# Kernel optimization log

Hardware: AMD Instinct MI355X
Metric: run time of the kernel (lower is better)

Reference implementation:

```python
import jax, jax.numpy as jnp
import numpy as np

B, L, D, N, F, V, NL, NS = 2, 1024, 768, 16, 3072, 32000, 4, 3
EPS = 1e-5


def _layernorm(x, g, b):
    m = x.mean(-1, keepdims=True)
    v = ((x - m) ** 2).mean(-1, keepdims=True)
    return (x - m) / jnp.sqrt(v + EPS) * g + b


def _ssm_sublayer(x, cw, A_log, WB, WC, Wdt, dtb, Dsk):
    # x: [B,L,D]; causal depthwise conv, kernel_size=3
    xp = jnp.pad(x, ((0, 0), (2, 0), (0, 0)))
    u = xp[:, :-2] * cw[:, 0] + xp[:, 1:-1] * cw[:, 1] + xp[:, 2:] * cw[:, 2]
    u = jax.nn.silu(u)
    dt = jax.nn.softplus(jnp.einsum('bld,de->ble', u, Wdt) + dtb)   # [B,L,D]
    Bm = jnp.einsum('bld,dn->bln', u, WB)                           # [B,L,N]
    Cm = jnp.einsum('bld,dn->bln', u, WC)                           # [B,L,N]
    A = -jnp.exp(A_log)                                             # [D,N]

    def step(h, t):
        dt_t, u_t, b_t, c_t = t                                     # [B,D],[B,D],[B,N],[B,N]
        h = jnp.exp(dt_t[..., None] * A) * h + (dt_t * u_t)[..., None] * b_t[:, None, :]
        y = jnp.einsum('bdn,bn->bd', h, c_t)
        return h, y

    h0 = jnp.zeros((x.shape[0], x.shape[2], A.shape[1]), x.dtype)
    _, ys = jax.lax.scan(step, h0, (dt.transpose(1, 0, 2), u.transpose(1, 0, 2),
                                    Bm.transpose(1, 0, 2), Cm.transpose(1, 0, 2)))
    return ys.transpose(1, 0, 2) + Dsk * u


def setup_inputs() -> dict:
    key = jax.random.key(0)
    ks = jax.random.split(key, 16)
    g = lambda k, shape, s=0.02: jax.random.normal(k, shape, jnp.float32) * s
    inp = {
        'x': jax.random.randint(ks[0], (B, L), 0, V),
        'emb': g(ks[1], (V, D)),
        'conv_w': g(ks[2], (NL, NS, D, 3), 0.2),
        'A_log': jnp.log(jnp.tile(jnp.arange(1, N + 1, dtype=jnp.float32), (NL, NS, D, 1))),
        'W_B': g(ks[3], (NL, NS, D, N)),
        'W_C': g(ks[4], (NL, NS, D, N)),
        'W_dt': g(ks[5], (NL, NS, D, D)),
        'dt_bias': jnp.full((NL, NS, D), -4.0, jnp.float32),
        'D_skip': jnp.ones((NL, NS, D), jnp.float32),
        'ffn_W1': g(ks[6], (NL, D, F)),
        'ffn_b1': jnp.zeros((NL, F), jnp.float32),
        'ffn_W2': g(ks[7], (NL, F, D)),
        'ffn_b2': jnp.zeros((NL, D), jnp.float32),
        'norm_g': jnp.ones((D,), jnp.float32),
        'norm_b': jnp.zeros((D,), jnp.float32),
        'out_W': g(ks[8], (D, V)),
        'out_b': jnp.zeros((V,), jnp.float32),
    }
    return inp


def reference(x, emb, conv_w, A_log, W_B, W_C, W_dt, dt_bias, D_skip,
              ffn_W1, ffn_b1, ffn_W2, ffn_b2, norm_g, norm_b, out_W, out_b):
    h = emb[x]                                                      # [B,L,D]
    for l in range(NL):
        for s in range(NS):
            h = h + _ssm_sublayer(h, conv_w[l, s], A_log[l, s], W_B[l, s],
                                  W_C[l, s], W_dt[l, s], dt_bias[l, s], D_skip[l, s])
        f = jax.nn.gelu(jnp.einsum('bld,df->blf', h, ffn_W1[l]) + ffn_b1[l], approximate=False)
        h = h + jnp.einsum('blf,fd->bld', f, ffn_W2[l]) + ffn_b2[l]
    h = _layernorm(h, norm_g, norm_b)
    logits = jnp.einsum('bld,dv->blv', h, out_W) + out_b            # [B,L,V]
    return logits
```

## Files before the change

### kernel.cpp

```cpp
#include <hip/hip_runtime.h>
#include <hip/hip_bf16.h>
#include <math.h>

#define BB 2
#define LL 1024
#define DD 768
#define NN 16
#define FF 3072
#define VV 32000
#define NLL 4
#define NSS 3
#define BL (BB*LL)
#define CHK 64
#define CLEN (LL/CHK)

typedef __bf16 bf16x8 __attribute__((ext_vector_type(8)));
typedef float f32x4 __attribute__((ext_vector_type(4)));
typedef short short8 __attribute__((ext_vector_type(8)));
typedef short short4v __attribute__((ext_vector_type(4)));

typedef __attribute__((address_space(1))) const void gconst_t;
typedef __attribute__((address_space(3))) void lds_t;

__device__ __forceinline__ void g2l16(const void* g, void* l) {
  __builtin_amdgcn_global_load_lds((gconst_t*)g, (lds_t*)l, 16, 0, 0);
}



__global__ __launch_bounds__(256) void k_embed(
    const int* __restrict__ x, const float* __restrict__ emb,
    float* __restrict__ h) {
  int gid = blockIdx.x * 256 + threadIdx.x;
  int row = gid / 192;
  int g = (gid - row * 192) * 4;
  int idx = x[row];
  *(float4*)&h[(size_t)row * DD + g] =
      *(const float4*)&emb[(size_t)idx * DD + g];
}

__global__ __launch_bounds__(256) void k_conv(
    const float* __restrict__ h, const float* __restrict__ cw,
    __hip_bfloat16* __restrict__ ub) {
  int gid = blockIdx.x * 256 + threadIdx.x;
  int row = gid / 192;
  int g = gid - row * 192;
  int d0 = g * 4;
  int l = row & (LL - 1);
  float4 h0 = *(const float4*)&h[(size_t)row * DD + d0];
  float4 h1, h2;
  if (l >= 1) h1 = *(const float4*)&h[(size_t)(row - 1) * DD + d0];
  else { h1.x = h1.y = h1.z = h1.w = 0.f; }
  if (l >= 2) h2 = *(const float4*)&h[(size_t)(row - 2) * DD + d0];
  else { h2.x = h2.y = h2.z = h2.w = 0.f; }
  const float* hp0 = (const float*)&h0;
  const float* hp1 = (const float*)&h1;
  const float* hp2 = (const float*)&h2;
  alignas(8) __hip_bfloat16 o[4];
  #pragma unroll
  for (int i = 0; i < 4; ++i) {
    int d = d0 + i;
    float v = hp2[i] * cw[d * 3 + 0] + hp1[i] * cw[d * 3 + 1] + hp0[i] * cw[d * 3 + 2];
    float sv = v / (1.f + __expf(-v));
    o[i] = __float2bfloat16(sv);
  }
  *(short4v*)&ub[(size_t)row * DD + d0] = *(short4v*)o;
}

__global__ __launch_bounds__(256) void k_layernorm(
    const float* __restrict__ x, const float* __restrict__ g,
    const float* __restrict__ bta, __hip_bfloat16* __restrict__ o) {
  int row = blockIdx.x;
  const float* xr = x + (size_t)row * DD;
  int tid = threadIdx.x;
  float v1 = xr[tid], v2 = xr[tid + 256], v3 = xr[tid + 512];
  float s = v1 + v2 + v3;
  float sq = v1 * v1 + v2 * v2 + v3 * v3;
  #pragma unroll
  for (int m = 1; m < 64; m <<= 1) {
    s  += __shfl_xor(s, m);
    sq += __shfl_xor(sq, m);
  }
  __shared__ float ss[4], sqs[4];
  if ((tid & 63) == 0) { ss[tid >> 6] = s; sqs[tid >> 6] = sq; }
  __syncthreads();
  s  = ss[0] + ss[1] + ss[2] + ss[3];
  sq = sqs[0] + sqs[1] + sqs[2] + sqs[3];
  float mean = s * (1.f / DD);
  float var  = sq * (1.f / DD) - mean * mean;
  float rstd = rsqrtf(var + 1e-5f);
  o[(size_t)row * DD + tid]       = __float2bfloat16((v1 - mean) * rstd * g[tid]       + bta[tid]);
  o[(size_t)row * DD + tid + 256] = __float2bfloat16((v2 - mean) * rstd * g[tid + 256] + bta[tid + 256]);
  o[(size_t)row * DD + tid + 512] = __float2bfloat16((v3 - mean) * rstd * g[tid + 512] + bta[tid + 512]);
}

#define S1 1728
#define S2 1740
#define S3 4044
#define S4 6348
#define SEND 12348

__global__ __launch_bounds__(256) void k_wconv_all(
    const float* __restrict__ Wdt, const float* __restrict__ WB,
    const float* __restrict__ WC, const float* __restrict__ W1,
    const float* __restrict__ W2, const float* __restrict__ Wout,
    __hip_bfloat16* __restrict__ WTdt, __hip_bfloat16* __restrict__ WT1,
    __hip_bfloat16* __restrict__ WT2, __hip_bfloat16* __restrict__ WTlog) {
  __shared__ float T[64][65];
  int bid = blockIdx.x;
  int tid = threadIdx.x;

  if (bid >= S1 && bid < S2) {
    int sub = bid - S1;
    const float* WBp = WB + (size_t)sub * DD * NN;
    const float* WCp = WC + (size_t)sub * DD * NN;
    __hip_bfloat16* dst = WTdt + (size_t)sub * 832 * DD;
    for (int e = tid; e < 64 * DD; e += 256) {
      int r = e / DD, k = e - (e / DD) * DD;
      float v = 0.f;
      if (r < 16)      v = WBp[(size_t)k * NN + r];
      else if (r < 32) v = WCp[(size_t)k * NN + (r - 16)];
      dst[(size_t)(768 + r) * DD + k] = __float2bfloat16(v);
    }
    return;
  }

  const float* W; __hip_bfloat16* WT;
  int K, N, n0, k0;
  if (bid < S1) {
    int sub = bid / 144, t = bid % 144;
    W = Wdt + (size_t)sub * DD * DD; WT = WTdt + (size_t)sub * 832 * DD;
    K = DD; N = DD; n0 = (t % 12) * 64; k0 = (t / 12) * 64;
  } else if (bid < S3) {
    int idx = bid - S2, l = idx / 576, t = idx % 576;
    W = W1 + (size_t)l * DD * FF; WT = WT1 + (size_t)l * FF * DD;
    K = DD; N = FF; n0 = (t % 48) * 64; k0 = (t / 48) * 64;
  } else if (bid < S4) {
    int idx = bid - S3, l = idx / 576, t = idx % 576;
    W = W2 + (size_t)l * FF * DD; WT = WT2 + (size_t)l * DD * FF;
    K = FF; N = DD; n0 = (t % 12) * 64; k0 = (t / 12) * 64;
  } else {
    int t = bid - S4;
    W = Wout; WT = WTlog;
    K = DD; N = VV; n0 = (t % 500) * 64; k0 = (t / 500) * 64;
  }

  {
    int r0 = tid >> 4, c4 = (tid & 15) * 4;
    #pragma unroll
    for (int i = 0; i < 4; ++i) {
      int r = r0 + 16 * i;
      float4 v = *(const float4*)&W[(size_t)(k0 + r) * N + n0 + c4];
      T[r][c4 + 0] = v.x;
      T[r][c4 + 1] = v.y;
      T[r][c4 + 2] = v.z;
      T[r][c4 + 3] = v.w;
    }
  }
  __syncthreads();
  {
    int c8 = tid & 7;
    #pragma unroll
    for (int j = 0; j < 2; ++j) {
      int n_l = (tid >> 3) + 32 * j;
      alignas(16) __hip_bfloat16 ox[8];
      #pragma unroll
      for (int i = 0; i < 8; ++i)
        ox[i] = __float2bfloat16(T[c8 * 8 + i][n_l]);
      *(short8*)&WT[(size_t)(n0 + n_l) * K + k0 + c8 * 8] = *(short8*)ox;
    }
  }
}

__device__ __forceinline__ float softplus_f(float x) {
  return (x > 20.f) ? x : log1pf(__expf(x));
}
__device__ __forceinline__ float gelu_f(float x) {
  return 0.5f * x * (1.f + erff(x * 0.70710678118654752f));
}

__global__ __launch_bounds__(256) void k_gemm_ffn1(
    const __hip_bfloat16* __restrict__ A, const __hip_bfloat16* __restrict__ BT,
    const float* __restrict__ bias, __hip_bfloat16* __restrict__ Cb) {
  __shared__ __align__(16) __hip_bfloat16 As[128 * 64];
  __shared__ __align__(16) __hip_bfloat16 Bs[128 * 64];
  const int tid = threadIdx.x;
  const int lane = tid & 63, wid = tid >> 6;
  int wg = (blockIdx.x & 7) * 48 + (blockIdx.x >> 3);
  int tn = wg % 24, tm = wg / 24;
  const int bm = tm * 128, bn = tn * 128;
  const int wm = wid >> 1, wn = wid & 1;
  const int sr = lane >> 3;
  const int sks = (((lane & 7) ^ (lane >> 3)) & 7) * 8;
  const int N = FF, K = DD;

  f32x4 acc[4][4] = {};

  for (int k0 = 0; k0 < K; k0 += 64) {
    __syncthreads();
    #pragma unroll
    for (int cc = 0; cc < 4; ++cc) {
      int ch = wid * 4 + cc;
      int row = ch * 8 + sr;
      g2l16(A  + (size_t)(bm + row) * K + k0 + sks, &As[ch * 512]);
      g2l16(BT + (size_t)(bn + row) * K + k0 + sks, &Bs[ch * 512]);
    }
    __syncthreads();
    #pragma unroll
    for (int kk = 0; kk < 2; ++kk) {
      int koff = (((kk * 4 + (lane >> 4)) ^ (lane & 7)) & 7) * 8;
      bf16x8 af[4], bfr[4];
      #pragma unroll
      for (int m = 0; m < 4; ++m)
        af[m] = *(const bf16x8*)&As[(wm * 64 + m * 16 + (lane & 15)) * 64 + koff];
      #pragma unroll
      for (int n = 0; n < 4; ++n)
        bfr[n] = *(const bf16x8*)&Bs[(wn * 64 + n * 16 + (lane & 15)) * 64 + koff];
      #pragma unroll
      for (int m = 0; m < 4; ++m)
        #pragma unroll
        for (int n = 0; n < 4; ++n)
          acc[m][n] = __builtin_amdgcn_mfma_f32_16x16x32_bf16(af[m], bfr[n], acc[m][n], 0, 0, 0);
    }
  }

  const int crow0 = (lane >> 4) * 4;
  const int ccol = lane & 15;
  #pragma unroll
  for (int m = 0; m < 4; ++m) {
    #pragma unroll
    for (int n = 0; n < 4; ++n) {
      int col = bn + wn * 64 + n * 16 + ccol;
      float bv = bias[col];
      #pragma unroll
      for (int j = 0; j < 4; ++j) {
        int row = bm + wm * 64 + m * 16 + crow0 + j;
        Cb[(size_t)row * N + col] = __float2bfloat16(gelu_f(acc[m][n][j] + bv));
      }
    }
  }
}

__global__ __launch_bounds__(256) void k_gemm_dtbc64(
    const __hip_bfloat16* __restrict__ A, const __hip_bfloat16* __restrict__ BT,
    const float* __restrict__ dtbias, __hip_bfloat16* __restrict__ dtbb,
    float* __restrict__ Bm, float* __restrict__ Cm) {
  __shared__ __align__(16) __hip_bfloat16 As[64 * 64];
  __shared__ __align__(16) __hip_bfloat16 Bs[64 * 64];
  const int tid = threadIdx.x;
  const int lane = tid & 63, wid = tid >> 6;
  int wg = (blockIdx.x & 7) * 52 + (blockIdx.x >> 3);
  int tn = wg % 13, tm = wg / 13;
  const int bm = tm * 64, bn = tn * 64;
  const int wm = wid >> 1, wn = wid & 1;
  const int sr = lane >> 3;
  const int sks = (((lane & 7) ^ (lane >> 3)) & 7) * 8;

  f32x4 acc[2][2] = {};

  for (int k0 = 0; k0 < DD; k0 += 64) {
    __syncthreads();
    #pragma unroll
    for (int cc = 0; cc < 2; ++cc) {
      int ch = wid * 2 + cc;
      int row = ch * 8 + sr;
      g2l16(A  + (size_t)(bm + row) * DD + k0 + sks, &As[ch * 512]);
      g2l16(BT + (size_t)(bn + row) * DD + k0 + sks, &Bs[ch * 512]);
    }
    __syncthreads();
    #pragma unroll
    for (int kk = 0; kk < 2; ++kk) {
      int koff = (((kk * 4 + (lane >> 4)) ^ (lane & 7)) & 7) * 8;
      bf16x8 af[2], bfr[2];
      #pragma unroll
      for (int m = 0; m < 2; ++m)
        af[m] = *(const bf16x8*)&As[(wm * 32 + m * 16 + (lane & 15)) * 64 + koff];
      #pragma unroll
      for (int n = 0; n < 2; ++n)
        bfr[n] = *(const bf16x8*)&Bs[(wn * 32 + n * 16 + (lane & 15)) * 64 + koff];
      #pragma unroll
      for (int m = 0; m < 2; ++m)
        #pragma unroll
        for (int n = 0; n < 2; ++n)
          acc[m][n] = __builtin_amdgcn_mfma_f32_16x16x32_bf16(af[m], bfr[n], acc[m][n], 0, 0, 0);
    }
  }

  const int crow0 = (lane >> 4) * 4;
  const int ccol = lane & 15;
  #pragma unroll
  for (int m = 0; m < 2; ++m) {
    #pragma unroll
    for (int n = 0; n < 2; ++n) {
      int col = bn + wn * 32 + n * 16 + ccol;
      if (col >= 800) continue;
      float bv = (col < DD) ? dtbias[col] : 0.f;
      #pragma unroll
      for (int j = 0; j < 4; ++j) {
        int row = bm + wm * 32 + m * 16 + crow0 + j;
        float v = acc[m][n][j] + bv;
        if (col < DD)       dtbb[(size_t)row * DD + col] = __float2bfloat16(softplus_f(v));
        else if (col < 784) Bm[(size_t)row * NN + (col - DD)] = v;
        else                Cm[(size_t)row * NN + (col - 784)] = v;
      }
    }
  }
}

__global__ __launch_bounds__(256) void k_gemm_ffn2s(
    const __hip_bfloat16* __restrict__ A, const __hip_bfloat16* __restrict__ BT,
    const float* __restrict__ bias, float* __restrict__ h) {
  __shared__ __align__(16) __hip_bfloat16 As[64 * 64];
  __shared__ __align__(16) __hip_bfloat16 Bs[64 * 64];
  const int tid = threadIdx.x;
  const int lane = tid & 63, wid = tid >> 6;
  int wg = (blockIdx.x & 7) * 96 + (blockIdx.x >> 3);
  int tile = wg % 384, split = wg / 384;
  int tm = tile % 32, tn = tile / 32;
  const int bm = tm * 64, bn = tn * 64;
  const int wm = wid >> 1, wn = wid & 1;
  const int sr = lane >> 3;
  const int sks = (((lane & 7) ^ (lane >> 3)) & 7) * 8;
  const int kbeg = split * (FF / 2), kend = kbeg + FF / 2;

  f32x4 acc[2][2] = {};

  for (int k0 = kbeg; k0 < kend; k0 += 64) {
    __syncthreads();
    #pragma unroll
    for (int cc = 0; cc < 2; ++cc) {
      int ch = wid * 2 + cc;
      int row = ch * 8 + sr;
      g2l16(A  + (size_t)(bm + row) * FF + k0 + sks, &As[ch * 512]);
      g2l16(BT + (size_t)(bn + row) * FF + k0 + sks, &Bs[ch * 512]);
    }
    __syncthreads();
    #pragma unroll
    for (int kk = 0; kk < 2; ++kk) {
      int koff = (((kk * 4 + (lane >> 4)) ^ (lane & 7)) & 7) * 8;
      bf16x8 af[2], bfr[2];
      #pragma unroll
      for (int m = 0; m < 2; ++m)
        af[m] = *(const bf16x8*)&As[(wm * 32 + m * 16 + (lane & 15)) * 64 + koff];
      #pragma unroll
      for (int n = 0; n < 2; ++n)
        bfr[n] = *(const bf16x8*)&Bs[(wn * 32 + n * 16 + (lane & 15)) * 64 + koff];
      #pragma unroll
      for (int m = 0; m < 2; ++m)
        #pragma unroll
        for (int n = 0; n < 2; ++n)
          acc[m][n] = __builtin_amdgcn_mfma_f32_16x16x32_bf16(af[m], bfr[n], acc[m][n], 0, 0, 0);
    }
  }

  const int crow0 = (lane >> 4) * 4;
  const int ccol = lane & 15;
  #pragma unroll
  for (int m = 0; m < 2; ++m) {
    #pragma unroll
    for (int n = 0; n < 2; ++n) {
      int col = bn + wn * 32 + n * 16 + ccol;
      float bv = (split == 0) ? bias[col] : 0.f;
      #pragma unroll
      for (int j = 0; j < 4; ++j) {
        int row = bm + wm * 32 + m * 16 + crow0 + j;
        unsafeAtomicAdd(&h[(size_t)row * DD + col], acc[m][n][j] + bv);
      }
    }
  }
}

__global__ __launch_bounds__(512) void k_gemm_logits2(
    const __hip_bfloat16* __restrict__ A, const __hip_bfloat16* __restrict__ BT,
    const float* __restrict__ bias, float* __restrict__ C, int M, int N, int K) {
  __shared__ __align__(16) char smem[(256 * 64 + 128 * 64) * 2];
  __hip_bfloat16* As = (__hip_bfloat16*)smem;
  __hip_bfloat16* Bs = (__hip_bfloat16*)(smem + 256 * 64 * 2);
  const int tid = threadIdx.x;
  const int lane = tid & 63, wid = tid >> 6;
  int bid = blockIdx.y * gridDim.x + blockIdx.x;
  int mt = bid & 7, nt = bid >> 3;
  const int bm = mt * 256, bn = nt * 128;
  const int wm = wid >> 1, wn = wid & 1;
  const int sr = lane >> 3;
  const int sks = (((lane & 7) ^ (lane >> 3)) & 7) * 8;

  f32x4 acc[4][4] = {};

  for (int k0 = 0; k0 < K; k0 += 64) {
    __syncthreads();
    #pragma unroll
    for (int r = 0; r < 4; ++r) {
      int ch = r * 8 + wid;
      int row = ch * 8 + sr;
      g2l16(A + (size_t)(bm + row) * K + k0 + sks, &As[ch * 512]);
    }
    #pragma unroll
    for (int r = 0; r < 2; ++r) {
      int ch = r * 8 + wid;
      int row = ch * 8 + sr;
      g2l16(BT + (size_t)(bn + row) * K + k0 + sks, &Bs[ch * 512]);
    }
    __syncthreads();
    #pragma unroll
    for (int kk = 0; kk < 2; ++kk) {
      int koff = (((kk * 4 + (lane >> 4)) ^ (lane & 7)) & 7) * 8;
      bf16x8 af[4], bfr[4];
      #pragma unroll
      for (int m = 0; m < 4; ++m)
        af[m] = *(const bf16x8*)&As[(wm * 64 + m * 16 + (lane & 15)) * 64 + koff];
      #pragma unroll
      for (int n = 0; n < 4; ++n)
        bfr[n] = *(const bf16x8*)&Bs[(wn * 64 + n * 16 + (lane & 15)) * 64 + koff];
      #pragma unroll
      for (int m = 0; m < 4; ++m)
        #pragma unroll
        for (int n = 0; n < 4; ++n)
          acc[m][n] = __builtin_amdgcn_mfma_f32_16x16x32_bf16(af[m], bfr[n], acc[m][n], 0, 0, 0);
    }
  }

  __syncthreads();
  float* eps = (float*)smem + (size_t)wid * 1088;
  const int crow0 = (lane >> 4) * 4;
  const int ccol = lane & 15;
  const int gcolbase = bn + wn * 64;
  #pragma unroll
  for (int m = 0; m < 4; ++m) {
    #pragma unroll
    for (int n = 0; n < 4; ++n) {
      float bv = bias[gcolbase + n * 16 + ccol];
      #pragma unroll
      for (int j = 0; j < 4; ++j)
        eps[(crow0 + j) * 68 + n * 16 + ccol] = acc[m][n][j] + bv;
    }
    int growbase = bm + wm * 64 + m * 16;
    #pragma unroll
    for (int p = 0; p < 2; ++p) {
      int r = (lane >> 3) + 8 * p;
      #pragma unroll
      for (int i = 0; i < 2; ++i) {
        int s4 = (lane & 7) + 8 * i;
        float4 v = *(float4*)&eps[r * 68 + s4 * 4];
        *(float4*)&C[(size_t)(growbase + r) * N + gcolbase + s4 * 4] = v;
      }
    }
  }
}

__global__ __launch_bounds__(256) void k_scan_a(
    const __hip_bfloat16* __restrict__ dt, const __hip_bfloat16* __restrict__ ub,
    const float* __restrict__ Bm, const float* __restrict__ A_log,
    __hip_bfloat16* __restrict__ F, float* __restrict__ SD) {
  int c = blockIdx.x;
  int bd = blockIdx.y;
  int b = bd / 3;
  int d = (bd % 3) * 256 + threadIdx.x;
  float Av[16];
  {
    const float4* al = (const float4*)(A_log + (size_t)d * NN);
    #pragma unroll
    for (int q = 0; q < 4; ++q) {
      float4 v = al[q];
      Av[q * 4 + 0] = -__expf(v.x);
      Av[q * 4 + 1] = -__expf(v.y);
      Av[q * 4 + 2] = -__expf(v.z);
      Av[q * 4 + 3] = -__expf(v.w);
    }
  }
  float h[16];
  #pragma unroll
  for (int n = 0; n < 16; ++n) h[n] = 0.f;
  float sdt = 0.f;
  size_t base = ((size_t)b * LL + (size_t)c * CLEN) * DD + d;
  int row0 = c * CLEN + b * LL;
  #pragma unroll 4
  for (int t = 0; t < CLEN; ++t) {
    float dtv = __bfloat162float(dt[base + (size_t)t * DD]);
    float uv  = __bfloat162float(ub[base + (size_t)t * DD]);
    float Bv[16];
    const float4* bp = (const float4*)(Bm + (size_t)(row0 + t) * NN);
    *(float4*)&Bv[0]  = bp[0];
    *(float4*)&Bv[4]  = bp[1];
    *(float4*)&Bv[8]  = bp[2];
    *(float4*)&Bv[12] = bp[3];
    float du = dtv * uv;
    sdt += dtv;
    #pragma unroll
    for (int n = 0; n < 16; ++n)
      h[n] = __expf(dtv * Av[n]) * h[n] + du * Bv[n];
  }
  alignas(16) __hip_bfloat16 fx[16];
  #pragma unroll
  for (int n = 0; n < 16; ++n) fx[n] = __float2bfloat16(h[n]);
  __hip_bfloat16* fo = F + (((size_t)c * BB + b) * DD + d) * NN;
  *(short8*)&fo[0] = *(short8*)&fx[0];
  *(short8*)&fo[8] = *(short8*)&fx[8];
  SD[((size_t)c * BB + b) * DD + d] = sdt;
}

__global__ __launch_bounds__(256) void k_scan_b(
    const __hip_bfloat16* __restrict__ F, const float* __restrict__ SD,
    const float* __restrict__ A_log, __hip_bfloat16* __restrict__ Hinit) {
  __shared__ float Ls[64 * 17];
  __shared__ float Ho[64 * 17];
  __shared__ float Ss[64];
  int bd = blockIdx.x;
  int b = bd / DD, d = bd % DD;
  int tid = threadIdx.x;
  if (tid < 128) {
    int c = tid >> 1, q = tid & 1;
    alignas(16) __hip_bfloat16 fx[8];
    *(short8*)fx = *(const short8*)(F + (((size_t)c * BB + b) * DD + d) * NN + q * 8);
    #pragma unroll
    for (int i = 0; i < 8; ++i)
      Ls[c * 17 + q * 8 + i] = __bfloat162float(fx[i]);
  }
  if (tid < 64) Ss[tid] = SD[((size_t)tid * BB + b) * DD + d];
  __syncthreads();
  int lane = tid & 63, w = tid >> 6;
  #pragma unroll
  for (int r = 0; r < 4; ++r) {
    int n = w * 4 + r;
    float Av = -__expf(A_log[(size_t)d * NN + n]);
    float Fv = Ls[lane * 17 + n];
    float Dv = __expf(Ss[lane] * Av);
    #pragma unroll
    for (int s = 1; s < 64; s <<= 1) {
      float Fp = __shfl_up(Fv, s);
      float Dp = __shfl_up(Dv, s);
      float nF = Fv + Dv * Fp;
      float nD = Dv * Dp;
      Fv = (lane >= s) ? nF : Fv;
      Dv = (lane >= s) ? nD : Dv;
    }
    float Hi = __shfl_up(Fv, 1);
    if (lane == 0) Hi = 0.f;
    Ho[lane * 17 + n] = Hi;
  }
  __syncthreads();
  if (tid < 128) {
    int c = tid >> 1, q = tid & 1;
    alignas(16) __hip_bfloat16 hx[8];
    #pragma unroll
    for (int i = 0; i < 8; ++i)
      hx[i] = __float2bfloat16(Ho[c * 17 + q * 8 + i]);
    *(short8*)(Hinit + (((size_t)c * BB + b) * DD + d) * NN + q * 8) = *(short8*)hx;
  }
}

__global__ __launch_bounds__(256) void k_scan_c(
    const __hip_bfloat16* __restrict__ dt, const __hip_bfloat16* __restrict__ ub,
    const float* __restrict__ Bm, const float* __restrict__ Cm,
    const float* __restrict__ A_log, const float* __restrict__ Dsk,
    const __hip_bfloat16* __restrict__ Hinit, float* __restrict__ hres,
    __hip_bfloat16* __restrict__ hb, int writeHb) {
  int c = blockIdx.x;
  int bd = blockIdx.y;
  int b = bd / 3;
  int d = (bd % 3) * 256 + threadIdx.x;
  float Av[16];
  {
    const float4* al = (const float4*)(A_log + (size_t)d * NN);
    #pragma unroll
    for (int q = 0; q < 4; ++q) {
      float4 v = al[q];
      Av[q * 4 + 0] = -__expf(v.x);
      Av[q * 4 + 1] = -__expf(v.y);
      Av[q * 4 + 2] = -__expf(v.z);
      Av[q * 4 + 3] = -__expf(v.w);
    }
  }
  float h[16];
  {
    alignas(16) __hip_bfloat16 hx[16];
    const __hip_bfloat16* hi = Hinit + (((size_t)c * BB + b) * DD + d) * NN;
    *(short8*)&hx[0] = *(const short8*)&hi[0];
    *(short8*)&hx[8] = *(const short8*)&hi[8];
    #pragma unroll
    for (int n = 0; n < 16; ++n) h[n] = __bfloat162float(hx[n]);
  }
  float dskip = Dsk[d];
  size_t base = ((size_t)b * LL + (size_t)c * CLEN) * DD + d;
  int row0 = c * CLEN + b * LL;
  #pragma unroll 4
  for (int t = 0; t < CLEN; ++t) {
    float dtv = __bfloat162float(dt[base + (size_t)t * DD]);
    float uv  = __bfloat162float(ub[base + (size_t)t * DD]);
    float Bv[16], Cv[16];
    const float4* bp = (const float4*)(Bm + (size_t)(row0 + t) * NN);
    const float4* cp = (const float4*)(Cm + (size_t)(row0 + t) * NN);
    *(float4*)&Bv[0]  = bp[0];
    *(float4*)&Bv[4]  = bp[1];
    *(float4*)&Bv[8]  = bp[2];
    *(float4*)&Bv[12] = bp[3];
    *(float4*)&Cv[0]  = cp[0];
    *(float4*)&Cv[4]  = cp[1];
    *(float4*)&Cv[8]  = cp[2];
    *(float4*)&Cv[12] = cp[3];
    float du = dtv * uv;
    float y = 0.f;
    #pragma unroll
    for (int n = 0; n < 16; ++n) {
      h[n] = __expf(dtv * Av[n]) * h[n] + du * Bv[n];
      y += h[n] * Cv[n];
    }
    float nh = hres[base + (size_t)t * DD] + y + dskip * uv;
    hres[base + (size_t)t * DD] = nh;
    if (writeHb) hb[base + (size_t)t * DD] = __float2bfloat16(nh);
  }
}

extern "C" void kernel_launch(void* const* d_in, const int* in_sizes, int n_in,
                              void* d_out, int out_size, void* d_ws, size_t ws_size,
                              hipStream_t stream) {
  const int*   x     = (const int*)d_in[0];
  const float* emb   = (const float*)d_in[1];
  const float* convw = (const float*)d_in[2];
  const float* A_log = (const float*)d_in[3];
  const float* W_B   = (const float*)d_in[4];
  const float* W_C   = (const float*)d_in[5];
  const float* W_dt  = (const float*)d_in[6];
  const float* dt_b  = (const float*)d_in[7];
  const float* D_sk  = (const float*)d_in[8];
  const float* W1    = (const float*)d_in[9];
  const float* b1    = (const float*)d_in[10];
  const float* W2    = (const float*)d_in[11];
  const float* b2    = (const float*)d_in[12];
  const float* ng    = (const float*)d_in[13];
  const float* nb    = (const float*)d_in[14];
  const float* Wout  = (const float*)d_in[15];
  const float* bout  = (const float*)d_in[16];
  float* out = (float*)d_out;

  __hip_bfloat16* WTdt = (__hip_bfloat16*)d_out;
  __hip_bfloat16* WT1  = WTdt + (size_t)12 * 832 * DD;
  __hip_bfloat16* WT2  = WT1  + (size_t)NLL * FF * DD;

  char* p = (char*)d_ws;
  auto alloc = [&](size_t bytes) { char* r = p; p += (bytes + 255) & ~(size_t)255; return r; };
  float* h    = (float*)alloc((size_t)BL * DD * 4);
  float* Bm   = (float*)alloc((size_t)BL * NN * 4);
  float* Cm   = (float*)alloc((size_t)BL * NN * 4);
  float* SD   = (float*)alloc((size_t)CHK * BB * DD * 4);
  __hip_bfloat16* dtbb  = (__hip_bfloat16*)alloc((size_t)BL * DD * 2);
  __hip_bfloat16* F     = (__hip_bfloat16*)alloc((size_t)CHK * BB * DD * NN * 2);
  __hip_bfloat16* Hini  = (__hip_bfloat16*)alloc((size_t)CHK * BB * DD * NN * 2);
  __hip_bfloat16* ub    = (__hip_bfloat16*)alloc((size_t)BL * DD * 2);
  __hip_bfloat16* hb    = (__hip_bfloat16*)alloc((size_t)BL * DD * 2);
  __hip_bfloat16* fb    = (__hip_bfloat16*)alloc((size_t)BL * FF * 2);
  __hip_bfloat16* lnb   = (__hip_bfloat16*)alloc((size_t)BL * DD * 2);
  __hip_bfloat16* WTlog = (__hip_bfloat16*)alloc((size_t)VV * DD * 2);

  k_wconv_all<<<SEND, 256, 0, stream>>>(
      W_dt, W_B, W_C, W1, W2, Wout, WTdt, WT1, WT2, WTlog);
  k_embed<<<1536, 256, 0, stream>>>(x, emb, h);

  for (int l = 0; l < NLL; ++l) {
    for (int s = 0; s < NSS; ++s) {
      int ls = l * NSS + s;
      k_conv<<<1536, 256, 0, stream>>>(h, convw + (size_t)ls * DD * 3, ub);
      k_gemm_dtbc64<<<416, 256, 0, stream>>>(
          ub, WTdt + (size_t)ls * 832 * DD, dt_b + (size_t)ls * DD, dtbb, Bm, Cm);
      k_scan_a<<<dim3(CHK, 6), 256, 0, stream>>>(
          dtbb, ub, Bm, A_log + (size_t)ls * DD * NN, F, SD);
      k_scan_b<<<BB * DD, 256, 0, stream>>>(
          F, SD, A_log + (size_t)ls * DD * NN, Hini);
      k_scan_c<<<dim3(CHK, 6), 256, 0, stream>>>(
          dtbb, ub, Bm, Cm, A_log + (size_t)ls * DD * NN, D_sk + (size_t)ls * DD,
          Hini, h, hb, (s == NSS - 1) ? 1 : 0);
    }
    k_gemm_ffn1<<<384, 256, 0, stream>>>(
        hb, WT1 + (size_t)l * FF * DD, b1 + (size_t)l * FF, fb);
    k_gemm_ffn2s<<<768, 256, 0, stream>>>(
        fb, WT2 + (size_t)l * DD * FF, b2 + (size_t)l * DD, h);
  }

  k_layernorm<<<BL, 256, 0, stream>>>(h, ng, nb, lnb);
  k_gemm_logits2<<<dim3(VV / 128, BL / 256), 512, 0, stream>>>(
      lnb, WTlog, bout, out, BL, VV, DD);
}
```

Baseline: 1.119 ms.

## Fuse three chunked-scan kernels into one cooperative kernel with grid syncs

Merges the chunk-local scan, cross-chunk prefix scan, and final scan passes into a single cooperative kernel of 384 blocks separated by grid-wide barriers, replacing two kernel launch boundaries per sublayer. The middle phase is re-mapped so each wavefront handles one (batch, channel) pair with 16 state elements per lane instead of one block per pair. This removes launch overhead and lets A values stay in registers across phases, at the cost of grid.sync overhead and reliance on all blocks being co-resident.

Measured after the change: 3.369 ms. 201% more time.

```diff
diff --git a/kernel.cpp b/kernel.cpp
--- a/kernel.cpp
+++ b/kernel.cpp
@@ -1,6 +1,9 @@
 #include <hip/hip_runtime.h>
 #include <hip/hip_bf16.h>
+#include <hip/hip_cooperative_groups.h>
 #include <math.h>
+
+namespace cg = cooperative_groups;
 
 #define BB 2
 #define LL 1024
@@ -448,14 +451,21 @@
   }
 }
 
-__global__ __launch_bounds__(256) void k_scan_a(
+__global__ __launch_bounds__(256) void k_scan_fused(
     const __hip_bfloat16* __restrict__ dt, const __hip_bfloat16* __restrict__ ub,
-    const float* __restrict__ Bm, const float* __restrict__ A_log,
-    __hip_bfloat16* __restrict__ F, float* __restrict__ SD) {
-  int c = blockIdx.x;
-  int bd = blockIdx.y;
-  int b = bd / 3;
-  int d = (bd % 3) * 256 + threadIdx.x;
+    const float* __restrict__ Bm, const float* __restrict__ Cm,
+    const float* __restrict__ A_log, const float* __restrict__ Dsk,
+    __hip_bfloat16* __restrict__ F, float* __restrict__ SD,
+    __hip_bfloat16* __restrict__ Hinit, float* __restrict__ hres,
+    __hip_bfloat16* __restrict__ hb, int writeHb) {
+  cg::grid_group grid = cg::this_grid();
+  int blk = blockIdx.x;
+  int tid = threadIdx.x;
+  int c = blk & 63;
+  int seg = blk >> 6;
+  int b = seg / 3;
+  int d = (seg % 3) * 256 + tid;
+
   float Av[16];
   {
     const float4* al = (const float4*)(A_log + (size_t)d * NN);
@@ -468,146 +478,136 @@
       Av[q * 4 + 3] = -__expf(v.w);
     }
   }
-  float h[16];
-  #pragma unroll
-  for (int n = 0; n < 16; ++n) h[n] = 0.f;
-  float sdt = 0.f;
-  size_t base = ((size_t)b * LL + (size_t)c * CLEN) * DD + d;
-  int row0 = c * CLEN + b * LL;
-  #pragma unroll 4
-  for (int t = 0; t < CLEN; ++t) {
-    float dtv = __bfloat162float(dt[base + (size_t)t * DD]);
-    float uv  = __bfloat162float(ub[base + (size_t)t * DD]);
-    float Bv[16];
-    const float4* bp = (const float4*)(Bm + (size_t)(row0 + t) * NN);
-    *(float4*)&Bv[0]  = bp[0];
-    *(float4*)&Bv[4]  = bp[1];
-    *(float4*)&Bv[8]  = bp[2];
-    *(float4*)&Bv[12] = bp[3];
-    float du = dtv * uv;
-    sdt += dtv;
-    #pragma unroll
-    for (int n = 0; n < 16; ++n)
-      h[n] = __expf(dtv * Av[n]) * h[n] + du * Bv[n];
-  }
-  alignas(16) __hip_bfloat16 fx[16];
-  #pragma unroll
-  for (int n = 0; n < 16; ++n) fx[n] = __float2bfloat16(h[n]);
-  __hip_bfloat16* fo = F + (((size_t)c * BB + b) * DD + d) * NN;
-  *(short8*)&fo[0] = *(short8*)&fx[0];
-  *(short8*)&fo[8] = *(short8*)&fx[8];
-  SD[((size_t)c * BB + b) * DD + d] = sdt;
-}
-
-__global__ __launch_bounds__(256) void k_scan_b(
-    const __hip_bfloat16* __restrict__ F, const float* __restrict__ SD,
-    const float* __restrict__ A_log, __hip_bfloat16* __restrict__ Hinit) {
-  __shared__ float Ls[64 * 17];
-  __shared__ float Ho[64 * 17];
-  __shared__ float Ss[64];
-  int bd = blockIdx.x;
-  int b = bd / DD, d = bd % DD;
-  int tid = threadIdx.x;
-  if (tid < 128) {
-    int c = tid >> 1, q = tid & 1;
-    alignas(16) __hip_bfloat16 fx[8];
-    *(short8*)fx = *(const short8*)(F + (((size_t)c * BB + b) * DD + d) * NN + q * 8);
-    #pragma unroll
-    for (int i = 0; i < 8; ++i)
-      Ls[c * 17 + q * 8 + i] = __bfloat162float(fx[i]);
-  }
-  if (tid < 64) Ss[tid] = SD[((size_t)tid * BB + b) * DD + d];
-  __syncthreads();
-  int lane = tid & 63, w = tid >> 6;
-  #pragma unroll
-  for (int r = 0; r < 4; ++r) {
-    int n = w * 4 + r;
-    float Av = -__expf(A_log[(size_t)d * NN + n]);
-    float Fv = Ls[lane * 17 + n];
-    float Dv = __expf(Ss[lane] * Av);
-    #pragma unroll
-    for (int s = 1; s < 64; s <<= 1) {
-      float Fp = __shfl_up(Fv, s);
-      float Dp = __shfl_up(Dv, s);
-      float nF = Fv + Dv * Fp;
-      float nD = Dv * Dp;
-      Fv = (lane >= s) ? nF : Fv;
-      Dv = (lane >= s) ? nD : Dv;
-    }
-    float Hi = __shfl_up(Fv, 1);
-    if (lane == 0) Hi = 0.f;
-    Ho[lane * 17 + n] = Hi;
-  }
-  __syncthreads();
-  if (tid < 128) {
-    int c = tid >> 1, q = tid & 1;
-    alignas(16) __hip_bfloat16 hx[8];
-    #pragma unroll
-    for (int i = 0; i < 8; ++i)
-      hx[i] = __float2bfloat16(Ho[c * 17 + q * 8 + i]);
-    *(short8*)(Hinit + (((size_t)c * BB + b) * DD + d) * NN + q * 8) = *(short8*)hx;
-  }
-}
-
-__global__ __launch_bounds__(256) void k_scan_c(
-    const __hip_bfloat16* __restrict__ dt, const __hip_bfloat16* __restrict__ ub,
-    const float* __restrict__ Bm, const float* __restrict__ Cm,
-    const float* __restrict__ A_log, const float* __restrict__ Dsk,
-    const __hip_bfloat16* __restrict__ Hinit, float* __restrict__ hres,
-    __hip_bfloat16* __restrict__ hb, int writeHb) {
-  int c = blockIdx.x;
-  int bd = blockIdx.y;
-  int b = bd / 3;
-  int d = (bd % 3) * 256 + threadIdx.x;
-  float Av[16];
+
   {
-    const float4* al = (const float4*)(A_log + (size_t)d * NN);
-    #pragma unroll
-    for (int q = 0; q < 4; ++q) {
-      float4 v = al[q];
-      Av[q * 4 + 0] = -__expf(v.x);
-      Av[q * 4 + 1] = -__expf(v.y);
-      Av[q * 4 + 2] = -__expf(v.z);
-      Av[q * 4 + 3] = -__expf(v.w);
-    }
-  }
-  float h[16];
+    float hA[16];
+    #pragma unroll
+    for (int n = 0; n < 16; ++n) hA[n] = 0.f;
+    float sdt = 0.f;
+    size_t base = ((size_t)b * LL + (size_t)c * CLEN) * DD + d;
+    int row0 = c * CLEN + b * LL;
+    #pragma unroll 4
+    for (int t = 0; t < CLEN; ++t) {
+      float dtv = __bfloat162float(dt[base + (size_t)t * DD]);
+      float uv  = __bfloat162float(ub[base + (size_t)t * DD]);
+      float Bv[16];
+      const float4* bp = (const float4*)(Bm + (size_t)(row0 + t) * NN);
+      *(float4*)&Bv[0]  = bp[0];
+      *(float4*)&Bv[4]  = bp[1];
+      *(float4*)&Bv[8]  = bp[2];
+      *(float4*)&Bv[12] = bp[3];
+      float du = dtv * uv;
+      sdt += dtv;
+      #pragma unroll
+      for (int n = 0; n < 16; ++n)
+        hA[n] = __expf(dtv * Av[n]) * hA[n] + du * Bv[n];
+    }
+    alignas(16) __hip_bfloat16 fx[16];
+    #pragma unroll
+    for (int n = 0; n < 16; ++n) fx[n] = __float2bfloat16(hA[n]);
+    __hip_bfloat16* fo = F + (((size_t)c * BB + b) * DD + d) * NN;
+    *(short8*)&fo[0] = *(short8*)&fx[0];
+    *(short8*)&fo[8] = *(short8*)&fx[8];
+    SD[((size_t)c * BB + b) * DD + d] = sdt;
+  }
+
+  __threadfence();
+  grid.sync();
+
   {
-    alignas(16) __hip_bfloat16 hx[16];
-    const __hip_bfloat16* hi = Hinit + (((size_t)c * BB + b) * DD + d) * NN;
-    *(short8*)&hx[0] = *(const short8*)&hi[0];
-    *(short8*)&hx[8] = *(const short8*)&hi[8];
-    #pragma unroll
-    for (int n = 0; n < 16; ++n) h[n] = __bfloat162float(hx[n]);
-  }
-  float dskip = Dsk[d];
-  size_t base = ((size_t)b * LL + (size_t)c * CLEN) * DD + d;
-  int row0 = c * CLEN + b * LL;
-  #pragma unroll 4
-  for (int t = 0; t < CLEN; ++t) {
-    float dtv = __bfloat162float(dt[base + (size_t)t * DD]);
-    float uv  = __bfloat162float(ub[base + (size_t)t * DD]);
-    float Bv[16], Cv[16];
-    const float4* bp = (const float4*)(Bm + (size_t)(row0 + t) * NN);
-    const float4* cp = (const float4*)(Cm + (size_t)(row0 + t) * NN);
-    *(float4*)&Bv[0]  = bp[0];
-    *(float4*)&Bv[4]  = bp[1];
-    *(float4*)&Bv[8]  = bp[2];
-    *(float4*)&Bv[12] = bp[3];
-    *(float4*)&Cv[0]  = cp[0];
-    *(float4*)&Cv[4]  = cp[1];
-    *(float4*)&Cv[8]  = cp[2];
-    *(float4*)&Cv[12] = cp[3];
-    float du = dtv * uv;
-    float y = 0.f;
+    int w = tid >> 6, lane = tid & 63;
+    int task = blk * 4 + w;
+    int b2 = task / DD, d2 = task - b2 * DD;
+    float Av2[16];
+    {
+      const float4* al = (const float4*)(A_log + (size_t)d2 * NN);
+      #pragma unroll
+      for (int q = 0; q < 4; ++q) {
+        float4 v = al[q];
+        Av2[q * 4 + 0] = -__expf(v.x);
+        Av2[q * 4 + 1] = -__expf(v.y);
+        Av2[q * 4 + 2] = -__expf(v.z);
+        Av2[q * 4 + 3] = -__expf(v.w);
+      }
+    }
+    float sd = SD[((size_t)lane * BB + b2) * DD + d2];
+    float Fr[16], Hr[16];
+    {
+      alignas(16) __hip_bfloat16 fx[16];
+      const __hip_bfloat16* fp = F + (((size_t)lane * BB + b2) * DD + d2) * NN;
+      *(short8*)&fx[0] = *(const short8*)&fp[0];
+      *(short8*)&fx[8] = *(const short8*)&fp[8];
+      #pragma unroll
+      for (int n = 0; n < 16; ++n) Fr[n] = __bfloat162float(fx[n]);
+    }
     #pragma unroll
     for (int n = 0; n < 16; ++n) {
-      h[n] = __expf(dtv * Av[n]) * h[n] + du * Bv[n];
-      y += h[n] * Cv[n];
-    }
-    float nh = hres[base + (size_t)t * DD] + y + dskip * uv;
-    hres[base + (size_t)t * DD] = nh;
-    if (writeHb) hb[base + (size_t)t * DD] = __float2bfloat16(nh);
+      float Fv = Fr[n];
+      float Dv = __expf(sd * Av2[n]);
+      #pragma unroll
+      for (int s = 1; s < 64; s <<= 1) {
+        float Fp = __shfl_up(Fv, s);
+        float Dp = __shfl_up(Dv, s);
+        float nF = Fv + Dv * Fp;
+        float nD = Dv * Dp;
+        Fv = (lane >= s) ? nF : Fv;
+        Dv = (lane >= s) ? nD : Dv;
+      }
+      float Hi = __shfl_up(Fv, 1);
+      Hr[n] = (lane == 0) ? 0.f : Hi;
+    }
+    {
+      alignas(16) __hip_bfloat16 hx[16];
+      #pragma unroll
+      for (int n = 0; n < 16; ++n) hx[n] = __float2bfloat16(Hr[n]);
+      __hip_bfloat16* hp = Hinit + (((size_t)lane * BB + b2) * DD + d2) * NN;
+      *(short8*)&hp[0] = *(short8*)&hx[0];
+      *(short8*)&hp[8] = *(short8*)&hx[8];
+    }
+  }
+
+  __threadfence();
+  grid.sync();
+
+  {
+    float hC[16];
+    {
+      alignas(16) __hip_bfloat16 hx[16];
+      const __hip_bfloat16* hi = Hinit + (((size_t)c * BB + b) * DD + d) * NN;
+      *(short8*)&hx[0] = *(const short8*)&hi[0];
+      *(short8*)&hx[8] = *(const short8*)&hi[8];
+      #pragma unroll
+      for (int n = 0; n < 16; ++n) hC[n] = __bfloat162float(hx[n]);
+    }
+    float dskip = Dsk[d];
+    size_t base = ((size_t)b * LL + (size_t)c * CLEN) * DD + d;
+    int row0 = c * CLEN + b * LL;
+    #pragma unroll 4
+    for (int t = 0; t < CLEN; ++t) {
+      float dtv = __bfloat162float(dt[base + (size_t)t * DD]);
+      float uv  = __bfloat162float(ub[base + (size_t)t * DD]);
+      float Bv[16], Cv[16];
+      const float4* bp = (const float4*)(Bm + (size_t)(row0 + t) * NN);
+      const float4* cp = (const float4*)(Cm + (size_t)(row0 + t) * NN);
+      *(float4*)&Bv[0]  = bp[0];
+      *(float4*)&Bv[4]  = bp[1];
+      *(float4*)&Bv[8]  = bp[2];
+      *(float4*)&Bv[12] = bp[3];
+      *(float4*)&Cv[0]  = cp[0];
+      *(float4*)&Cv[4]  = cp[1];
+      *(float4*)&Cv[8]  = cp[2];
+      *(float4*)&Cv[12] = cp[3];
+      float du = dtv * uv;
+      float y = 0.f;
+      #pragma unroll
+      for (int n = 0; n < 16; ++n) {
+        hC[n] = __expf(dtv * Av[n]) * hC[n] + du * Bv[n];
+        y += hC[n] * Cv[n];
+      }
+      float nh = hres[base + (size_t)t * DD] + y + dskip * uv;
+      hres[base + (size_t)t * DD] = nh;
+      if (writeHb) hb[base + (size_t)t * DD] = __float2bfloat16(nh);
+    }
   }
 }
 
@@ -662,13 +662,24 @@
       k_conv<<<1536, 256, 0, stream>>>(h, convw + (size_t)ls * DD * 3, ub);
       k_gemm_dtbc64<<<416, 256, 0, stream>>>(
           ub, WTdt + (size_t)ls * 832 * DD, dt_b + (size_t)ls * DD, dtbb, Bm, Cm);
-      k_scan_a<<<dim3(CHK, 6), 256, 0, stream>>>(
-          dtbb, ub, Bm, A_log + (size_t)ls * DD * NN, F, SD);
-      k_scan_b<<<BB * DD, 256, 0, stream>>>(
-          F, SD, A_log + (size_t)ls * DD * NN, Hini);
-      k_scan_c<<<dim3(CHK, 6), 256, 0, stream>>>(
-          dtbb, ub, Bm, Cm, A_log + (size_t)ls * DD * NN, D_sk + (size_t)ls * DD,
-          Hini, h, hb, (s == NSS - 1) ? 1 : 0);
+      {
+        const __hip_bfloat16* dt_p = dtbb;
+        const __hip_bfloat16* ub_p = ub;
+        const float* Bm_p   = Bm;
+        const float* Cm_p   = Cm;
+        const float* alog_p = A_log + (size_t)ls * DD * NN;
+        const float* dsk_p  = D_sk + (size_t)ls * DD;
+        __hip_bfloat16* F_p = F; float* SD_p = SD;
+        __hip_bfloat16* Hi_p = Hini;
+        float* h_p = h; __hip_bfloat16* hb_p = hb;
+        int wHb = (s == NSS - 1) ? 1 : 0;
+        void* args[] = {
+          (void*)&dt_p, (void*)&ub_p, (void*)&Bm_p, (void*)&Cm_p,
+          (void*)&alog_p, (void*)&dsk_p, (void*)&F_p, (void*)&SD_p,
+          (void*)&Hi_p, (void*)&h_p, (void*)&hb_p, (void*)&wHb};
+        hipLaunchCooperativeKernel((void*)k_scan_fused, dim3(CHK * 6), dim3(256),
+                                   args, 0, stream);
+      }
     }
     k_gemm_ffn1<<<384, 256, 0, stream>>>(
         hb, WT1 + (size_t)l * FF * DD, b1 + (size_t)l * FF, fb);
```
